# Kernel optimization log

Measured on AMD Instinct MI355X. Metric: run time of the kernel, lower is better.

Reference implementation:

```python
import jax, jax.numpy as jnp
import numpy as np

# ---- static configuration (mirrors module init kwargs) ----
RADIUS = 8.0
MAX_NEIGHBORS = 32          # max_num_neighbors_threshold
MAX_REP = (2, 2, 0)         # static: rep = min(ceil(radius*inv_min_dist), threshold) = 2 for a1,a2; pbc[2]=False -> 0
B, N_ATOMS = 32, 128
CELL_EDGE = 4.0


def _unit_cells():
    # torch.cartesian_prod over arange(-rep, rep+1) per dim; pbc z disabled -> single 0
    ax = [np.arange(-r, r + 1, dtype=np.float32) for r in MAX_REP]
    g = np.stack(np.meshgrid(*ax, indexing='ij'), axis=-1).reshape(-1, 3)
    return jnp.asarray(g)  # [C, 3], C = 5*5*1 = 25


def setup_inputs() -> dict:
    key = jax.random.key(0)
    k1, k2 = jax.random.split(key)
    # near-cubic cells ~4A with small perturbation (keeps rep clamped at threshold=2)
    cell = (CELL_EDGE * jnp.eye(3, dtype=jnp.float32)[None] +
            0.05 * jax.random.normal(k2, (B, 3, 3), dtype=jnp.float32))
    # atoms at fractional coords in [0,1): pos = frac @ cell
    frac = jax.random.uniform(k1, (B, N_ATOMS, 3), dtype=jnp.float32)
    pos = jnp.einsum('bnf,bfk->bnk', frac, cell)
    return {'pos': pos, 'cell': cell}


def reference(pos, cell):
    """PBC radius-graph construction (gen_edges_from_batch), padded form.

    Candidate edges live on a fixed grid [B, i, j, c]: i = index1 (center atom),
    j = index2 (neighbor), c = periodic image. Returns:
      edge_dist       [B,N,N,C] f32  distance (0 where edge invalid)
      edge_cell_type  [B,N,N,C] i32  linearized cell-offset id (0 where invalid)
      edge_mask       [B,N,N,C] bool edge survives radius + self + kNN truncation
      num_neighbors_image [B]   i32  per-image edge counts (clamped), as in torch
    """
    u = _unit_cells()                         # [C,3]
    C = u.shape[0]
    # pbc offsets: offset_c = u_c @ cell_b  (matches cell_offsets.bmm(cell))
    off = jnp.einsum('ci,bik->bck', u, cell)  # [B,C,3]

    # distance vectors: pos[index2] - pos[index1] + offset (get_pbc_distances convention)
    dvec = (pos[:, None, :, None, :] - pos[:, :, None, None, :]
            + off[:, None, None, :, :])       # [B,N,N,C,3]
    d2 = jnp.sum(dvec * dvec, axis=-1)        # [B,N,N,C]

    within = (d2 <= RADIUS * RADIUS) & (d2 > 1e-4)

    # --- sort-based neighbor truncation per center atom i (get_max_neighbors_mask) ---
    num_atoms = B * N_ATOMS
    rows = jnp.where(within, d2, jnp.inf).reshape(num_atoms, N_ATOMS * C)
    order = jnp.argsort(rows, axis=1)         # stable: ties keep (j,c) order as torch
    ranks = jnp.argsort(order, axis=1)        # inverse permutation = rank of each cand
    keep = (ranks < MAX_NEIGHBORS).reshape(B, N_ATOMS, N_ATOMS, C) & within

    # per-image clamped neighbor counts (segment_csr of clamped segment_coo)
    num_nb = jnp.sum(within, axis=(2, 3)).astype(jnp.int32)          # [B,N]
    num_neighbors_image = jnp.sum(jnp.minimum(num_nb, MAX_NEIGHBORS), axis=1)

    safe_d2 = jnp.where(keep, d2, 1.0)
    edge_dist = jnp.where(keep, jnp.sqrt(safe_d2), 0.0)

    # linearized cell type: (offsets + max_rep) . [nr1*nr2, nr1, 1] with nr = 2*rep+1
    nr = np.array([2 * r + 1 for r in MAX_REP])
    mults = jnp.asarray([nr[1] * nr[2], nr[1], 1], dtype=jnp.int32)  # matches torch code
    ct = jnp.sum((u.astype(jnp.int32) + jnp.asarray(MAX_REP, jnp.int32)) * mults, axis=-1)  # [C]
    edge_cell_type = jnp.where(keep, ct[None, None, None, :], 0).astype(jnp.int32)

    return edge_dist, edge_cell_type, keep, num_neighbors_image
```

## Files before the change

kernel.cpp:

```cpp
#include <hip/hip_runtime.h>
#include <math.h>
#include <stdint.h>

#define NATOMS   128
#define NCELLS   25
#define NCAND    (NATOMS * NCELLS)
#define MAXNB    32
#define R2       64.0f
#define BLK      256
#define KEYCAP   128

__global__ __launch_bounds__(BLK) void graph_kernel(
    const float* __restrict__ pos, const float* __restrict__ cell,
    float* __restrict__ out_dist, float* __restrict__ out_ctype,
    float* __restrict__ out_mask, float* __restrict__ ws_counts)
{
    __shared__ float4 s_pos4[NATOMS];
    __shared__ float4 s_off4[NCELLS];
    __shared__ float  s_ct[NCELLS];
    __shared__ float  s_ctr[3];
    __shared__ float  s_d2[NCAND];
    __shared__ unsigned s_hist[256];
    __shared__ unsigned s_wtot[4];
    __shared__ int s_wred[4];
    __shared__ unsigned long long s_keys[KEYCAP];
    __shared__ unsigned s_cnt;
    __shared__ int s_binsel, s_need, s_tot, s_att;
    __shared__ unsigned long long s_K;

    const int bi   = blockIdx.x;
    const int b    = bi >> 7;
    const int tid  = threadIdx.x;
    const int lane = tid & 63;
    const int w    = tid >> 6;

    if (tid < NATOMS) {
        const float* p = pos + (b * NATOMS + tid) * 3;
        s_pos4[tid] = make_float4(p[0], p[1], p[2], 0.0f);
    }
    if (tid >= NATOMS && tid < NATOMS + 3)
        s_ctr[tid - NATOMS] = pos[bi * 3 + (tid - NATOMS)];
    if (tid >= 160 && tid < 160 + NCELLS) {
        int c = tid - 160;
        float ux = (float)(c / 5 - 2);
        float uy = (float)(c % 5 - 2);
        float ox = __fadd_rn(__fmul_rn(ux, cell[b*9+0]), __fmul_rn(uy, cell[b*9+3]));
        float oy = __fadd_rn(__fmul_rn(ux, cell[b*9+1]), __fmul_rn(uy, cell[b*9+4]));
        float oz = __fadd_rn(__fmul_rn(ux, cell[b*9+2]), __fmul_rn(uy, cell[b*9+5]));
        s_off4[c] = make_float4(ox, oy, oz, 0.0f);
        s_ct[c] = (float)(5 * (c / 5) + 5 * (c % 5));
    }
    s_hist[tid] = 0u;
    if (tid == 0) { s_cnt = 0; s_binsel = -1; s_need = 0; s_att = 0; s_K = ~0ULL; }
    __syncthreads();

    const float cx = s_ctr[0], cy = s_ctr[1], cz = s_ctr[2];

    int local = 0;
    for (int g = tid; g < NCAND; g += BLK) {
        int c = g >> 7;
        int j = g & 127;
        float4 p = s_pos4[j];
        float4 o = s_off4[c];
        float dx = __fadd_rn(__fsub_rn(p.x, cx), o.x);
        float dy = __fadd_rn(__fsub_rn(p.y, cy), o.y);
        float dz = __fadd_rn(__fsub_rn(p.z, cz), o.z);
        float d2 = __fadd_rn(__fadd_rn(__fmul_rn(dx,dx), __fmul_rn(dy,dy)),
                             __fmul_rn(dz,dz));
        bool within = (d2 <= R2) && (d2 > 1e-4f);
        int f = j * NCELLS + c;
        s_d2[f] = within ? d2 : __builtin_inff();
        if (within) {
            local++;
            if (d2 < 16.0f)
                atomicAdd(&s_hist[(int)(d2 * 16.0f)], 1u);
        }
    }
    for (int o = 32; o; o >>= 1) local += __shfl_down(local, o);
    if (lane == 0) s_wred[w] = local;
    __syncthreads();
    if (tid == 0) {
        int tot = s_wred[0] + s_wred[1] + s_wred[2] + s_wred[3];
        s_tot = tot;
        ws_counts[bi] = (float)(tot < MAXNB ? tot : MAXNB);
    }
    __syncthreads();

    if (s_tot > MAXNB) {
        for (int att = 0; att < 2 && s_binsel < 0; att++) {
            if (att == 1) {
                s_hist[tid] = 0u;
                __syncthreads();
                for (int v = tid; v < NCAND / 4; v += BLK) {
                    float4 dq = ((const float4*)s_d2)[v];
                    #pragma unroll
                    for (int e = 0; e < 4; e++) {
                        float d2 = (&dq.x)[e];
                        if (d2 < 64.5f) {
                            int bin = (int)(d2 * 4.0f);
                            if (bin > 255) bin = 255;
                            atomicAdd(&s_hist[bin], 1u);
                        }
                    }
                }
                __syncthreads();
            }
            unsigned h = s_hist[tid];
            int v = (int)h;
            #pragma unroll
            for (int off = 1; off < 64; off <<= 1) {
                int u = __shfl_up(v, off, 64);
                if (lane >= off) v += u;
            }
            if (lane == 63) s_wtot[w] = (unsigned)v;
            __syncthreads();
            unsigned pre = 0;
            for (int ww = 0; ww < w; ww++) pre += s_wtot[ww];
            unsigned htot = s_wtot[0] + s_wtot[1] + s_wtot[2] + s_wtot[3];
            unsigned ci = (unsigned)v + pre, ce = ci - h;
            if (htot >= MAXNB && h > 0 && ce < MAXNB && ci >= MAXNB) {
                s_binsel = tid;
                s_need   = MAXNB - (int)ce;
                s_att    = att;
            }
            __syncthreads();
        }

        const int   binsel = s_binsel;
        const float sc  = s_att ? 4.0f  : 16.0f;
        const float lim = s_att ? 64.5f : 16.0f;
        for (int v = tid; v < NCAND / 4; v += BLK) {
            float4 dq = ((const float4*)s_d2)[v];
            #pragma unroll
            for (int e = 0; e < 4; e++) {
                float d2 = (&dq.x)[e];
                if (d2 < lim) {
                    int bin = (int)(d2 * sc);
                    if (bin > 255) bin = 255;
                    if (bin == binsel) {
                        unsigned idx = atomicAdd(&s_cnt, 1u);
                        if (idx < KEYCAP)
                            s_keys[idx] =
                                ((unsigned long long)__float_as_uint(d2) << 32)
                                | (unsigned)(v * 4 + e);
                    }
                }
            }
        }
        __syncthreads();
        const int m = (int)s_cnt, need = s_need;
        if (m <= KEYCAP) {
            for (int p = tid; p < m; p += BLK) {
                unsigned long long kp = s_keys[p];
                int r = 0;
                for (int q = 0; q < m; q++) r += (s_keys[q] < kp);
                if (r == need - 1) s_K = kp;
            }
        } else {
            for (int f = tid; f < NCAND; f += BLK) {
                float d2 = s_d2[f];
                if (d2 < lim) {
                    int bin = (int)(d2 * sc);
                    if (bin > 255) bin = 255;
                    if (bin == binsel) {
                        unsigned long long kf =
                            ((unsigned long long)__float_as_uint(d2) << 32) | (unsigned)f;
                        int r = 0;
                        for (int q = 0; q < NCAND; q++) {
                            float dq = s_d2[q];
                            if (dq < lim) {
                                int bq = (int)(dq * sc);
                                if (bq > 255) bq = 255;
                                if (bq == binsel) {
                                    unsigned long long kq =
                                        ((unsigned long long)__float_as_uint(dq) << 32)
                                        | (unsigned)q;
                                    r += (kq < kf);
                                }
                            }
                        }
                        if (r == need - 1) s_K = kf;
                    }
                }
            }
        }
        __syncthreads();
    }
    const unsigned long long K = s_K;

    const long long base = (long long)bi * NCAND;
    float4* o0 = (float4*)(out_dist  + base);
    float4* o1 = (float4*)(out_ctype + base);
    float4* o2 = (float4*)(out_mask  + base);
    for (int v = tid; v < NCAND / 4; v += BLK) {
        float4 dq = ((const float4*)s_d2)[v];
        int f0 = v * 4;
        int c0 = f0 % NCELLS;
        float4 r0, r1, r2;
        #pragma unroll
        for (int e = 0; e < 4; e++) {
            float d2 = (&dq.x)[e];
            int ce = c0 + e; if (ce >= NCELLS) ce -= NCELLS;
            bool within = (d2 <= R2);
            unsigned long long key =
                ((unsigned long long)__float_as_uint(d2) << 32) | (unsigned)(f0 + e);
            bool keep = within && (key <= K);
            (&r0.x)[e] = keep ? sqrtf(d2) : 0.0f;
            (&r1.x)[e] = keep ? s_ct[ce] : 0.0f;
            (&r2.x)[e] = keep ? 1.0f : 0.0f;
        }
        o0[v] = r0; o1[v] = r1; o2[v] = r2;
    }
}

__global__ __launch_bounds__(64) void reduce_counts(
    const float* __restrict__ ws_counts, float* __restrict__ out_nb)
{
    int b = blockIdx.x;
    int t = threadIdx.x;
    float v = ws_counts[b * NATOMS + t] + ws_counts[b * NATOMS + 64 + t];
    for (int o = 32; o; o >>= 1) v += __shfl_down(v, o);
    if (t == 0) out_nb[b] = v;
}

extern "C" void kernel_launch(void* const* d_in, const int* in_sizes, int n_in,
                              void* d_out, int out_size, void* d_ws, size_t ws_size,
                              hipStream_t stream) {
    const float* pos  = (const float*)d_in[0];
    const float* cell = (const float*)d_in[1];
    float* out = (float*)d_out;
    const long long E = 32LL * NATOMS * NATOMS * NCELLS;
    float* out_dist  = out;
    float* out_ct    = out + E;
    float* out_mask  = out + 2 * E;
    float* out_nb    = out + 3 * E;
    float* ws = (float*)d_ws;

    hipLaunchKernelGGL(graph_kernel, dim3(32 * NATOMS), dim3(BLK), 0, stream,
                       pos, cell, out_dist, out_ct, out_mask, ws);
    hipLaunchKernelGGL(reduce_counts, dim3(32), dim3(64), 0, stream,
                       ws, out_nb);
}
```

Before: 167.9 us.

## Keep per-thread distances in registers and fold count reduction into main kernel

Removes the 12.8KB shared-memory distance array: each thread now holds its 16 candidate squared distances in registers, laid out in the same contiguous groups of four it later writes. This cuts LDS use so more blocks can be resident, and drops the shared stores and reloads. The separate per-image count reduction kernel is replaced by a memset plus a float atomicAdd from each block. The overflow fallback now recomputes distances on the fly, and register pressure rises.

```diff
diff --git a/kernel.cpp b/kernel.cpp
--- a/kernel.cpp
+++ b/kernel.cpp
@@ -8,18 +8,17 @@
 #define MAXNB    32
 #define R2       64.0f
 #define BLK      256
-#define KEYCAP   128
+#define NGRP     (NCAND / 4)
+#define KEYCAP   256
 
 __global__ __launch_bounds__(BLK) void graph_kernel(
     const float* __restrict__ pos, const float* __restrict__ cell,
     float* __restrict__ out_dist, float* __restrict__ out_ctype,
-    float* __restrict__ out_mask, float* __restrict__ ws_counts)
+    float* __restrict__ out_mask, float* __restrict__ out_nb)
 {
     __shared__ float4 s_pos4[NATOMS];
     __shared__ float4 s_off4[NCELLS];
     __shared__ float  s_ct[NCELLS];
-    __shared__ float  s_ctr[3];
-    __shared__ float  s_d2[NCAND];
     __shared__ unsigned s_hist[256];
     __shared__ unsigned s_wtot[4];
     __shared__ int s_wred[4];
@@ -30,6 +29,7 @@
 
     const int bi   = blockIdx.x;
     const int b    = bi >> 7;
+    const int i    = bi & 127;
     const int tid  = threadIdx.x;
     const int lane = tid & 63;
     const int w    = tid >> 6;
@@ -38,8 +38,6 @@
         const float* p = pos + (b * NATOMS + tid) * 3;
         s_pos4[tid] = make_float4(p[0], p[1], p[2], 0.0f);
     }
-    if (tid >= NATOMS && tid < NATOMS + 3)
-        s_ctr[tid - NATOMS] = pos[bi * 3 + (tid - NATOMS)];
     if (tid >= 160 && tid < 160 + NCELLS) {
         int c = tid - 160;
         float ux = (float)(c / 5 - 2);
@@ -54,26 +52,35 @@
     if (tid == 0) { s_cnt = 0; s_binsel = -1; s_need = 0; s_att = 0; s_K = ~0ULL; }
     __syncthreads();
 
-    const float cx = s_ctr[0], cy = s_ctr[1], cz = s_ctr[2];
-
+    const float4 ctr = s_pos4[i];
+
+    float d2r[16];
     int local = 0;
-    for (int g = tid; g < NCAND; g += BLK) {
-        int c = g >> 7;
-        int j = g & 127;
-        float4 p = s_pos4[j];
-        float4 o = s_off4[c];
-        float dx = __fadd_rn(__fsub_rn(p.x, cx), o.x);
-        float dy = __fadd_rn(__fsub_rn(p.y, cy), o.y);
-        float dz = __fadd_rn(__fsub_rn(p.z, cz), o.z);
-        float d2 = __fadd_rn(__fadd_rn(__fmul_rn(dx,dx), __fmul_rn(dy,dy)),
-                             __fmul_rn(dz,dz));
-        bool within = (d2 <= R2) && (d2 > 1e-4f);
-        int f = j * NCELLS + c;
-        s_d2[f] = within ? d2 : __builtin_inff();
-        if (within) {
-            local++;
-            if (d2 < 16.0f)
-                atomicAdd(&s_hist[(int)(d2 * 16.0f)], 1u);
+    #pragma unroll
+    for (int k = 0; k < 4; k++) {
+        int g = k * BLK + tid;
+        if (g < NGRP) {
+            int f0 = g * 4;
+            int j = f0 / 25;
+            int c = f0 - j * 25;
+            #pragma unroll
+            for (int e = 0; e < 4; e++) {
+                float4 p = s_pos4[j];
+                float4 o = s_off4[c];
+                float dx = __fadd_rn(__fsub_rn(p.x, ctr.x), o.x);
+                float dy = __fadd_rn(__fsub_rn(p.y, ctr.y), o.y);
+                float dz = __fadd_rn(__fsub_rn(p.z, ctr.z), o.z);
+                float d2 = __fadd_rn(__fadd_rn(__fmul_rn(dx,dx), __fmul_rn(dy,dy)),
+                                     __fmul_rn(dz,dz));
+                bool within = (d2 <= R2) && (d2 > 1e-4f);
+                d2r[k*4+e] = within ? d2 : __builtin_inff();
+                if (within) {
+                    local++;
+                    if (d2 < 16.0f)
+                        atomicAdd(&s_hist[(int)(d2 * 16.0f)], 1u);
+                }
+                c++; if (c == 25) { c = 0; j++; }
+            }
         }
     }
     for (int o = 32; o; o >>= 1) local += __shfl_down(local, o);
@@ -82,7 +89,7 @@
     if (tid == 0) {
         int tot = s_wred[0] + s_wred[1] + s_wred[2] + s_wred[3];
         s_tot = tot;
-        ws_counts[bi] = (float)(tot < MAXNB ? tot : MAXNB);
+        atomicAdd(&out_nb[b], (float)(tot < MAXNB ? tot : MAXNB));
     }
     __syncthreads();
 
@@ -91,15 +98,18 @@
             if (att == 1) {
                 s_hist[tid] = 0u;
                 __syncthreads();
-                for (int v = tid; v < NCAND / 4; v += BLK) {
-                    float4 dq = ((const float4*)s_d2)[v];
-                    #pragma unroll
-                    for (int e = 0; e < 4; e++) {
-                        float d2 = (&dq.x)[e];
-                        if (d2 < 64.5f) {
-                            int bin = (int)(d2 * 4.0f);
-                            if (bin > 255) bin = 255;
-                            atomicAdd(&s_hist[bin], 1u);
+                #pragma unroll
+                for (int k = 0; k < 4; k++) {
+                    int g = k * BLK + tid;
+                    if (g < NGRP) {
+                        #pragma unroll
+                        for (int e = 0; e < 4; e++) {
+                            float d2 = d2r[k*4+e];
+                            if (d2 < 64.5f) {
+                                int bin = (int)(d2 * 4.0f);
+                                if (bin > 255) bin = 255;
+                                atomicAdd(&s_hist[bin], 1u);
+                            }
                         }
                     }
                 }
@@ -129,20 +139,24 @@
         const int   binsel = s_binsel;
         const float sc  = s_att ? 4.0f  : 16.0f;
         const float lim = s_att ? 64.5f : 16.0f;
-        for (int v = tid; v < NCAND / 4; v += BLK) {
-            float4 dq = ((const float4*)s_d2)[v];
-            #pragma unroll
-            for (int e = 0; e < 4; e++) {
-                float d2 = (&dq.x)[e];
-                if (d2 < lim) {
-                    int bin = (int)(d2 * sc);
-                    if (bin > 255) bin = 255;
-                    if (bin == binsel) {
-                        unsigned idx = atomicAdd(&s_cnt, 1u);
-                        if (idx < KEYCAP)
-                            s_keys[idx] =
-                                ((unsigned long long)__float_as_uint(d2) << 32)
-                                | (unsigned)(v * 4 + e);
+        #pragma unroll
+        for (int k = 0; k < 4; k++) {
+            int g = k * BLK + tid;
+            if (g < NGRP) {
+                int f0 = g * 4;
+                #pragma unroll
+                for (int e = 0; e < 4; e++) {
+                    float d2 = d2r[k*4+e];
+                    if (d2 < lim) {
+                        int bin = (int)(d2 * sc);
+                        if (bin > 255) bin = 255;
+                        if (bin == binsel) {
+                            unsigned idx = atomicAdd(&s_cnt, 1u);
+                            if (idx < KEYCAP)
+                                s_keys[idx] =
+                                    ((unsigned long long)__float_as_uint(d2) << 32)
+                                    | (unsigned)(f0 + e);
+                        }
                     }
                 }
             }
@@ -157,30 +171,42 @@
                 if (r == need - 1) s_K = kp;
             }
         } else {
-            for (int f = tid; f < NCAND; f += BLK) {
-                float d2 = s_d2[f];
-                if (d2 < lim) {
+            #pragma unroll 1
+            for (int k = 0; k < 4; k++) {
+                int g = k * BLK + tid;
+                if (g >= NGRP) continue;
+                int f0 = g * 4;
+                for (int e = 0; e < 4; e++) {
+                    float d2 = d2r[k*4+e];
+                    if (d2 >= lim) continue;
                     int bin = (int)(d2 * sc);
                     if (bin > 255) bin = 255;
-                    if (bin == binsel) {
-                        unsigned long long kf =
-                            ((unsigned long long)__float_as_uint(d2) << 32) | (unsigned)f;
-                        int r = 0;
-                        for (int q = 0; q < NCAND; q++) {
-                            float dq = s_d2[q];
-                            if (dq < lim) {
-                                int bq = (int)(dq * sc);
-                                if (bq > 255) bq = 255;
-                                if (bq == binsel) {
-                                    unsigned long long kq =
-                                        ((unsigned long long)__float_as_uint(dq) << 32)
-                                        | (unsigned)q;
-                                    r += (kq < kf);
-                                }
-                            }
-                        }
-                        if (r == need - 1) s_K = kf;
+                    if (bin != binsel) continue;
+                    unsigned long long kf =
+                        ((unsigned long long)__float_as_uint(d2) << 32)
+                        | (unsigned)(f0 + e);
+                    int r = 0;
+                    for (int q = 0; q < NCAND; q++) {
+                        int jq = q / 25, cq = q - (q / 25) * 25;
+                        float4 p = s_pos4[jq];
+                        float4 o = s_off4[cq];
+                        float dx = __fadd_rn(__fsub_rn(p.x, ctr.x), o.x);
+                        float dy = __fadd_rn(__fsub_rn(p.y, ctr.y), o.y);
+                        float dz = __fadd_rn(__fsub_rn(p.z, ctr.z), o.z);
+                        float dq = __fadd_rn(__fadd_rn(__fmul_rn(dx,dx),
+                                                       __fmul_rn(dy,dy)),
+                                             __fmul_rn(dz,dz));
+                        bool within = (dq <= R2) && (dq > 1e-4f);
+                        if (!within || dq >= lim) continue;
+                        int bq = (int)(dq * sc);
+                        if (bq > 255) bq = 255;
+                        if (bq != binsel) continue;
+                        unsigned long long kq =
+                            ((unsigned long long)__float_as_uint(dq) << 32)
+                            | (unsigned)q;
+                        r += (kq < kf);
                     }
+                    if (r == need - 1) s_K = kf;
                 }
             }
         }
@@ -192,35 +218,30 @@
     float4* o0 = (float4*)(out_dist  + base);
     float4* o1 = (float4*)(out_ctype + base);
     float4* o2 = (float4*)(out_mask  + base);
-    for (int v = tid; v < NCAND / 4; v += BLK) {
-        float4 dq = ((const float4*)s_d2)[v];
-        int f0 = v * 4;
-        int c0 = f0 % NCELLS;
-        float4 r0, r1, r2;
-        #pragma unroll
-        for (int e = 0; e < 4; e++) {
-            float d2 = (&dq.x)[e];
-            int ce = c0 + e; if (ce >= NCELLS) ce -= NCELLS;
-            bool within = (d2 <= R2);
-            unsigned long long key =
-                ((unsigned long long)__float_as_uint(d2) << 32) | (unsigned)(f0 + e);
-            bool keep = within && (key <= K);
-            (&r0.x)[e] = keep ? sqrtf(d2) : 0.0f;
-            (&r1.x)[e] = keep ? s_ct[ce] : 0.0f;
-            (&r2.x)[e] = keep ? 1.0f : 0.0f;
-        }
-        o0[v] = r0; o1[v] = r1; o2[v] = r2;
-    }
-}
-
-__global__ __launch_bounds__(64) void reduce_counts(
-    const float* __restrict__ ws_counts, float* __restrict__ out_nb)
-{
-    int b = blockIdx.x;
-    int t = threadIdx.x;
-    float v = ws_counts[b * NATOMS + t] + ws_counts[b * NATOMS + 64 + t];
-    for (int o = 32; o; o >>= 1) v += __shfl_down(v, o);
-    if (t == 0) out_nb[b] = v;
+    #pragma unroll
+    for (int k = 0; k < 4; k++) {
+        int g = k * BLK + tid;
+        if (g < NGRP) {
+            int f0 = g * 4;
+            int j = f0 / 25;
+            int c = f0 - j * 25;
+            float4 r0, r1, r2;
+            #pragma unroll
+            for (int e = 0; e < 4; e++) {
+                float d2 = d2r[k*4+e];
+                bool within = (d2 <= R2);
+                unsigned long long key =
+                    ((unsigned long long)__float_as_uint(d2) << 32)
+                    | (unsigned)(f0 + e);
+                bool keep = within && (key <= K);
+                (&r0.x)[e] = keep ? sqrtf(d2) : 0.0f;
+                (&r1.x)[e] = keep ? s_ct[c] : 0.0f;
+                (&r2.x)[e] = keep ? 1.0f : 0.0f;
+                c++; if (c == 25) c = 0;
+            }
+            o0[g] = r0; o1[g] = r1; o2[g] = r2;
+        }
+    }
 }
 
 extern "C" void kernel_launch(void* const* d_in, const int* in_sizes, int n_in,
@@ -234,10 +255,8 @@
     float* out_ct    = out + E;
     float* out_mask  = out + 2 * E;
     float* out_nb    = out + 3 * E;
-    float* ws = (float*)d_ws;
-
+
+    hipMemsetAsync(out_nb, 0, 32 * sizeof(float), stream);
     hipLaunchKernelGGL(graph_kernel, dim3(32 * NATOMS), dim3(BLK), 0, stream,
-                       pos, cell, out_dist, out_ct, out_mask, ws);
-    hipLaunchKernelGGL(reduce_counts, dim3(32), dim3(64), 0, stream,
-                       ws, out_nb);
+                       pos, cell, out_dist, out_ct, out_mask, out_nb);
 }
```

Measured after the change: 190.5 us. 1.13x slower.
